# Kernel optimization log

Measured on AMD Instinct MI355X. Metric: run time of the kernel, lower is better.

## Reference

```python
import jax, jax.numpy as jnp
import numpy as np

B, FH, N, TIN = 8, 8, 2048, 5      # batch(time for LSTM), f_length, nodes, in_length
H1, H2 = 32, 64                    # traj_linear_hidden, lstm_encoder_size
NEG = -9e15

def setup_inputs() -> dict:
    key = jax.random.key(0)
    ks = jax.random.split(key, 12)
    s = lambda k, shape, fan: jax.random.normal(k, shape, jnp.float32) * (1.0 / np.sqrt(fan))
    return {
        "hist": jax.random.normal(ks[0], (B, FH, N, TIN), jnp.float32),
        "adj": jax.random.randint(ks[1], (B, 2, N, N), 0, 2, jnp.int32),
        "W1": s(ks[2], (H1, TIN * FH), TIN * FH),
        "b1": jnp.zeros((H1,), jnp.float32),
        "W_ih": s(ks[3], (4 * H2, H1), H1),
        "W_hh": s(ks[4], (4 * H2, H2), H2),
        "b_ih": jnp.zeros((4 * H2,), jnp.float32),
        "b_hh": jnp.zeros((4 * H2,), jnp.float32),
        "Wg": s(ks[5], (H2, H2), H2),
        "a_src": s(ks[6], (H2,), H2),
        "a_dst": s(ks[7], (H2,), H2),
    }

def _lstm(x, W_ih, W_hh, b_ih, b_hh):
    # x: [T, Nb, H1] (torch nn.LSTM seq-first); gate order i,f,g,o
    Nb = x.shape[1]
    h0 = jnp.zeros((Nb, H2), x.dtype)
    c0 = jnp.zeros((Nb, H2), x.dtype)
    def step(carry, xt):
        h, c = carry
        g = xt @ W_ih.T + b_ih + h @ W_hh.T + b_hh        # [Nb, 4*H2]
        i, f, gg, o = jnp.split(g, 4, axis=-1)
        c = jax.nn.sigmoid(f) * c + jax.nn.sigmoid(i) * jnp.tanh(gg)
        h = jax.nn.sigmoid(o) * jnp.tanh(c)
        return (h, c), h
    _, hs = jax.lax.scan(step, (h0, c0), x)
    return hs                                              # [T, Nb, H2]

def reference(hist, adj, W1, b1, W_ih, W_hh, b_ih, b_hh, Wg, a_src, a_dst):
    # hist.permute(0,2,3,1).flatten(2,3) -> [B, N, TIN*FH]
    x = jnp.transpose(hist, (0, 2, 3, 1)).reshape(B, N, TIN * FH)
    h1 = jax.nn.elu(x @ W1.T + b1)                         # [B, N, H1]
    hs = _lstm(h1, W_ih, W_hh, b_ih, b_hh)                 # [B, N, H2]
    # GAT over adj[:, -1]
    A = adj[:, -1, :, :] > 0                               # [B, N, N]
    Wh = hs @ Wg                                           # [B, N, H2]
    e = jax.nn.leaky_relu(
        (Wh @ a_src)[:, :, None] + (Wh @ a_dst)[:, None, :], 0.2)
    e = jnp.where(A, e, NEG)
    alpha = jax.nn.softmax(e, axis=-1)                     # [B, N, N]
    out = jax.nn.elu(jnp.einsum("bij,bjd->bid", alpha, Wh))
    return out
```

## Files before the change

kernel.cpp:

```cpp
#include <hip/hip_runtime.h>
#include <hip/hip_bf16.h>
#include <math.h>

#define BB 8
#define FH 8
#define NN 2048
#define TIN 5
#define H1 32
#define H2 64

typedef const void* cvp;
typedef __attribute__((ext_vector_type(8))) short short8;
typedef __attribute__((ext_vector_type(4))) float floatx4;

__device__ __forceinline__ float ldx(cvp p, int i, int bf) {
  if (bf) return __bfloat162float(((const __hip_bfloat16*)p)[i]);
  return ((const float*)p)[i];
}

__device__ __forceinline__ float4 ld4(cvp p, int i, int bf) {
  if (bf) {
    const __hip_bfloat162* q = (const __hip_bfloat162*)p;
    float2 a = __bfloat1622float2(q[(i >> 1)]);
    float2 b = __bfloat1622float2(q[(i >> 1) + 1]);
    return make_float4(a.x, a.y, b.x, b.y);
  }
  return ((const float4*)p)[i >> 2];
}

__device__ __forceinline__ float sigf(float x) {
  return 1.f / (1.f + __expf(-x));
}

__global__ void k_detect(const unsigned int* __restrict__ w, int* __restrict__ flag) {
  __shared__ int cnt;
  if (threadIdx.x == 0) cnt = 0;
  __syncthreads();
  int local = 0;
  for (int i = threadIdx.x; i < 1024; i += 256) {
    unsigned e = (w[i] >> 7) & 0xFFu;
    local += (e >= 100u && e <= 150u) ? 1 : 0;
  }
  atomicAdd(&cnt, local);
  __syncthreads();
  if (threadIdx.x == 0) *flag = (cnt > 700) ? 1 : 0;
}

__global__ void k_h1(cvp hist, cvp W1, cvp b1, float* __restrict__ h1,
                     const int* __restrict__ flagp) {
  __shared__ float w[H1 * TIN * FH];
  __shared__ float bb[H1];
  int bf = *flagp;
  int tid = threadIdx.x;
  for (int i = tid; i < H1 * TIN * FH; i += 256) w[i] = ldx(W1, i, bf);
  if (tid < H1) bb[tid] = ldx(b1, tid, bf);
  __syncthreads();
  int t = blockIdx.x >> 8;
  int n = ((blockIdx.x & 255) << 3) + (tid >> 5);
  int k = tid & 31;
  float acc = bb[k];
#pragma unroll
  for (int ti = 0; ti < TIN; ++ti) {
#pragma unroll
    for (int f = 0; f < FH; ++f) {
      acc += ldx(hist, (((t * FH + f) * NN + n) * TIN) + ti, bf) *
             w[k * (TIN * FH) + ti * FH + f];
    }
  }
  h1[((t * NN + n) * H1) + k] = (acc > 0.f) ? acc : expm1f(acc);
}

__global__ __launch_bounds__(256, 2) void k_lstm(
    const float* __restrict__ h1, cvp W_ih, cvp W_hh, cvp b_ih, cvp b_hh,
    float* __restrict__ hs, const int* __restrict__ flagp) {
  __shared__ __align__(16) float xh[4][96];
  __shared__ float gbuf[4][256];
  int bf = *flagp;
  int tid = threadIdx.x;
  int w = tid >> 6, lane = tid & 63;
  int g = (w << 6) + lane;
  int n0 = blockIdx.x << 2;
  int node_w = n0 + w;

  float wreg[96];
#pragma unroll
  for (int kq = 0; kq < 8; ++kq) {
    float4 v = ld4(W_ih, g * 32 + (kq << 2), bf);
    wreg[(kq << 2) + 0] = v.x; wreg[(kq << 2) + 1] = v.y;
    wreg[(kq << 2) + 2] = v.z; wreg[(kq << 2) + 3] = v.w;
  }
#pragma unroll
  for (int kq = 0; kq < 16; ++kq) {
    float4 v = ld4(W_hh, g * 64 + (kq << 2), bf);
    wreg[32 + (kq << 2) + 0] = v.x; wreg[32 + (kq << 2) + 1] = v.y;
    wreg[32 + (kq << 2) + 2] = v.z; wreg[32 + (kq << 2) + 3] = v.w;
  }
  float bias = ldx(b_ih, g, bf) + ldx(b_hh, g, bf);

  xh[w][32 + lane] = 0.f;
  float c = 0.f;

  for (int t = 0; t < BB; ++t) {
    if (lane < 32) xh[w][lane] = h1[((t * NN + node_w) * H1) + lane];
    __syncthreads();
    float acc[4] = {bias, bias, bias, bias};
    const float4* xq0 = (const float4*)xh[0];
    const float4* xq1 = (const float4*)xh[1];
    const float4* xq2 = (const float4*)xh[2];
    const float4* xq3 = (const float4*)xh[3];
#pragma unroll
    for (int kq = 0; kq < 24; ++kq) {
      float w0 = wreg[(kq << 2) + 0], w1 = wreg[(kq << 2) + 1];
      float w2 = wreg[(kq << 2) + 2], w3 = wreg[(kq << 2) + 3];
      float4 v0 = xq0[kq], v1 = xq1[kq], v2 = xq2[kq], v3 = xq3[kq];
      acc[0] += w0 * v0.x + w1 * v0.y + w2 * v0.z + w3 * v0.w;
      acc[1] += w0 * v1.x + w1 * v1.y + w2 * v1.z + w3 * v1.w;
      acc[2] += w0 * v2.x + w1 * v2.y + w2 * v2.z + w3 * v2.w;
      acc[3] += w0 * v3.x + w1 * v3.y + w2 * v3.z + w3 * v3.w;
    }
#pragma unroll
    for (int nd = 0; nd < 4; ++nd) gbuf[nd][g] = acc[nd];
    __syncthreads();
    float gi = gbuf[w][lane];
    float gf = gbuf[w][64 + lane];
    float gg = gbuf[w][128 + lane];
    float go = gbuf[w][192 + lane];
    c = sigf(gf) * c + sigf(gi) * tanhf(gg);
    float h = sigf(go) * tanhf(c);
    xh[w][32 + lane] = h;
    hs[((t * NN + node_w) * H2) + lane] = h;
    __syncthreads();
  }
}

__global__ __launch_bounds__(256) void k_gatprep(
    const float* __restrict__ hs, cvp Wg, cvp a_src, cvp a_dst,
    __hip_bfloat16* __restrict__ WhFr, float* __restrict__ sv,
    float* __restrict__ dv, const int* __restrict__ flagp) {
  __shared__ float wg[H2 * H2];
  __shared__ float tile[32][H2 + 1];
  int bf = *flagp;
  int tid = threadIdx.x;
  for (int i = tid; i < H2 * H2; i += 256) wg[i] = ldx(Wg, i, bf);
  __syncthreads();
  int wave = tid >> 6, lane = tid & 63;
  int b = blockIdx.x >> 6;
  int jt = blockIdx.x & 63;
  int j0 = jt << 5;
  float as = ldx(a_src, lane, bf);
  float ad = ldx(a_dst, lane, bf);
#pragma unroll
  for (int rr = 0; rr < 8; ++rr) {
    int jl = (wave << 3) + rr;
    int row = b * NN + j0 + jl;
    float hreg = hs[row * H2 + lane];
    float acc = 0.f;
#pragma unroll
    for (int k = 0; k < H2; ++k)
      acc += __shfl(hreg, k, 64) * wg[(k << 6) + lane];
    tile[jl][lane] = acc;
    float s = acc * as, d = acc * ad;
#pragma unroll
    for (int off = 32; off > 0; off >>= 1) {
      s += __shfl_xor(s, off, 64);
      d += __shfl_xor(d, off, 64);
    }
    if (lane == 0) { sv[row] = s; dv[row] = d; }
  }
  __syncthreads();
  int nt = tid >> 6, l = tid & 63;
  int q = l >> 4, m = l & 15;
  float v[8];
#pragma unroll
  for (int jj = 0; jj < 8; ++jj)
    v[jj] = tile[(q << 3) + jj][(nt << 4) + m];
  short8 fr;
#pragma unroll
  for (int p = 0; p < 4; ++p)
    ((__hip_bfloat162*)&fr)[p] =
        __float22bfloat162_rn(make_float2(v[2 * p], v[2 * p + 1]));
  size_t off = ((size_t)(b * 64 + jt) * 4 + nt) * 64 + l;
  ((short8*)WhFr)[off] = fr;
}

struct Stage {
  int4 a0, a1;
  float4 d0, d1;
  short8 b0, b1, b2, b3;
};

__device__ __forceinline__ Stage ld_stage(const int* arow, const float* drow,
                                          const short8* wf, int ks, int k0, int lane) {
  Stage s;
  int kb = ks * 32 + k0;
  s.a0 = *(const int4*)(arow + kb);
  s.a1 = *(const int4*)(arow + kb + 4);
  s.d0 = *(const float4*)(drow + kb);
  s.d1 = *(const float4*)(drow + kb + 4);
  const short8* base = wf + (size_t)ks * 256 + lane;
  s.b0 = base[0];
  s.b1 = base[64];
  s.b2 = base[128];
  s.b3 = base[192];
  return s;
}

__global__ __launch_bounds__(256, 3) void k_gat(
    const int* __restrict__ adj, const __hip_bfloat16* __restrict__ WhFr,
    const float* __restrict__ sv, const float* __restrict__ dv,
    void* __restrict__ out, const int* __restrict__ flagp) {
  __shared__ floatx4 abuf[3][4][64];
  __shared__ float sbuf[3][64];
  int bf = *flagp;
  int tid = threadIdx.x;
  int w = tid >> 6, lane = tid & 63;
  int b = blockIdx.x >> 7;
  int i0 = (blockIdx.x & 127) << 4;
  int q = lane >> 4, m = lane & 15;
  int i = i0 + m;
  float sva = sv[b * NN + i];
  const int* arow = adj + ((size_t)(b * 2 + 1) * NN + i) * NN;
  const float* drow = dv + b * NN;
  const short8* wf = ((const short8*)WhFr) + (size_t)b * 64 * 256;
  floatx4 acc0 = {0.f, 0.f, 0.f, 0.f};
  floatx4 acc1 = acc0, acc2 = acc0, acc3 = acc0;
  float S = 0.f;
  int k0 = q << 3;
  int ksb = w << 4;

  Stage s0 = ld_stage(arow, drow, wf, ksb + 0, k0, lane);
  Stage s1 = ld_stage(arow, drow, wf, ksb + 1, k0, lane);
#pragma unroll 2
  for (int ks = 0; ks < 16; ++ks) {
    int ksn = ksb + ((ks + 2 < 16) ? ks + 2 : 15);
    Stage nx = ld_stage(arow, drow, wf, ksn, k0, lane);
    int av[8] = {s0.a0.x, s0.a0.y, s0.a0.z, s0.a0.w,
                 s0.a1.x, s0.a1.y, s0.a1.z, s0.a1.w};
    float dd[8] = {s0.d0.x, s0.d0.y, s0.d0.z, s0.d0.w,
                   s0.d1.x, s0.d1.y, s0.d1.z, s0.d1.w};
    float pv[8];
#pragma unroll
    for (int jj = 0; jj < 8; ++jj) {
      float t = sva + dd[jj];
      float e = __expf(fmaxf(t, 0.2f * t));
      float p = (av[jj] != 0) ? e : 0.f;
      pv[jj] = p;
      S += p;
    }
    short8 afr;
#pragma unroll
    for (int p2 = 0; p2 < 4; ++p2)
      ((__hip_bfloat162*)&afr)[p2] =
          __float22bfloat162_rn(make_float2(pv[2 * p2], pv[2 * p2 + 1]));
    acc0 = __builtin_amdgcn_mfma_f32_16x16x32_bf16(afr, s0.b0, acc0, 0, 0, 0);
    acc1 = __builtin_amdgcn_mfma_f32_16x16x32_bf16(afr, s0.b1, acc1, 0, 0, 0);
    acc2 = __builtin_amdgcn_mfma_f32_16x16x32_bf16(afr, s0.b2, acc2, 0, 0, 0);
    acc3 = __builtin_amdgcn_mfma_f32_16x16x32_bf16(afr, s0.b3, acc3, 0, 0, 0);
    s0 = s1;
    s1 = nx;
  }
  S += __shfl_xor(S, 16, 64);
  S += __shfl_xor(S, 32, 64);
  if (w > 0) {
    abuf[w - 1][0][lane] = acc0;
    abuf[w - 1][1][lane] = acc1;
    abuf[w - 1][2][lane] = acc2;
    abuf[w - 1][3][lane] = acc3;
    sbuf[w - 1][lane] = S;
  }
  __syncthreads();
  if (w != 0) return;
#pragma unroll
  for (int ww = 0; ww < 3; ++ww) {
    acc0 += abuf[ww][0][lane];
    acc1 += abuf[ww][1][lane];
    acc2 += abuf[ww][2][lane];
    acc3 += abuf[ww][3][lane];
    S += sbuf[ww][lane];
  }
  float inv = 1.f / S;
  float ivr[4];
#pragma unroll
  for (int r = 0; r < 4; ++r) ivr[r] = __shfl(inv, (q << 2) + r, 64);

  floatx4 accs[4] = {acc0, acc1, acc2, acc3};
  if (bf) {
    __hip_bfloat16* o = (__hip_bfloat16*)out;
#pragma unroll
    for (int nt = 0; nt < 4; ++nt) {
#pragma unroll
      for (int r = 0; r < 4; ++r) {
        float v = accs[nt][r] * ivr[r];
        v = (v > 0.f) ? v : expm1f(v);
        int row = i0 + (q << 2) + r;
        o[((size_t)b * NN + row) * H2 + (nt << 4) + m] = __float2bfloat16(v);
      }
    }
  } else {
    float* o = (float*)out;
#pragma unroll
    for (int nt = 0; nt < 4; ++nt) {
#pragma unroll
      for (int r = 0; r < 4; ++r) {
        float v = accs[nt][r] * ivr[r];
        v = (v > 0.f) ? v : expm1f(v);
        int row = i0 + (q << 2) + r;
        o[((size_t)b * NN + row) * H2 + (nt << 4) + m] = v;
      }
    }
  }
}

extern "C" void kernel_launch(void* const* d_in, const int* in_sizes, int n_in,
                              void* d_out, int out_size, void* d_ws, size_t ws_size,
                              hipStream_t stream) {
  (void)in_sizes; (void)n_in; (void)out_size; (void)ws_size;
  cvp hist  = d_in[0];
  const int* adj = (const int*)d_in[1];
  cvp W1    = d_in[2];
  cvp b1    = d_in[3];
  cvp W_ih  = d_in[4];
  cvp W_hh  = d_in[5];
  cvp b_ih  = d_in[6];
  cvp b_hh  = d_in[7];
  cvp Wg    = d_in[8];
  cvp a_src = d_in[9];
  cvp a_dst = d_in[10];

  float* ws  = (float*)d_ws;
  float* h1  = ws;
  float* hs  = h1 + BB * NN * H1;
  __hip_bfloat16* WhFr = (__hip_bfloat16*)(hs + BB * NN * H2);
  float* sv  = hs + BB * NN * H2 + 524288;
  float* dv  = sv + BB * NN;
  int* flag  = (int*)(dv + BB * NN);

  k_detect<<<1, 256, 0, stream>>>((const unsigned int*)W_ih, flag);
  k_h1<<<2048, 256, 0, stream>>>(hist, W1, b1, h1, flag);
  k_lstm<<<512, 256, 0, stream>>>(h1, W_ih, W_hh, b_ih, b_hh, hs, flag);
  k_gatprep<<<512, 256, 0, stream>>>(hs, Wg, a_src, a_dst, WhFr, sv, dv, flag);
  k_gat<<<1024, 256, 0, stream>>>(adj, WhFr, sv, dv, d_out, flag);
}
```

Baseline: 432.7 us.

## Fuse input projection into LSTM and bitmask adjacency with MFMA row-sum in GAT

Folds the first linear+ELU layer into the LSTM kernel, computing each timestep's 32-wide input from hist inside the block and dropping the h1 intermediate buffer and one launch. In the GAT kernel, each block first packs its 16 adjacency rows into shared-memory bitmasks via wave ballots and stages dv in shared memory. The main loop then reads mask bits and dv from LDS instead of streaming int4 adjacency per step. The softmax denominator moves to an extra MFMA against a ones vector, and occupancy is raised to 4 blocks. The costs are an extra barrier per LSTM step, a shallower prefetch pipeline in the GAT loop, and a row sum now taken over bf16-rounded probabilities.

After: 467.2 us. 8.0% more time.

```diff
diff --git a/kernel.cpp b/kernel.cpp
--- a/kernel.cpp
+++ b/kernel.cpp
@@ -46,35 +46,14 @@
   if (threadIdx.x == 0) *flag = (cnt > 700) ? 1 : 0;
 }
 
-__global__ void k_h1(cvp hist, cvp W1, cvp b1, float* __restrict__ h1,
-                     const int* __restrict__ flagp) {
-  __shared__ float w[H1 * TIN * FH];
-  __shared__ float bb[H1];
-  int bf = *flagp;
-  int tid = threadIdx.x;
-  for (int i = tid; i < H1 * TIN * FH; i += 256) w[i] = ldx(W1, i, bf);
-  if (tid < H1) bb[tid] = ldx(b1, tid, bf);
-  __syncthreads();
-  int t = blockIdx.x >> 8;
-  int n = ((blockIdx.x & 255) << 3) + (tid >> 5);
-  int k = tid & 31;
-  float acc = bb[k];
-#pragma unroll
-  for (int ti = 0; ti < TIN; ++ti) {
-#pragma unroll
-    for (int f = 0; f < FH; ++f) {
-      acc += ldx(hist, (((t * FH + f) * NN + n) * TIN) + ti, bf) *
-             w[k * (TIN * FH) + ti * FH + f];
-    }
-  }
-  h1[((t * NN + n) * H1) + k] = (acc > 0.f) ? acc : expm1f(acc);
-}
-
 __global__ __launch_bounds__(256, 2) void k_lstm(
-    const float* __restrict__ h1, cvp W_ih, cvp W_hh, cvp b_ih, cvp b_hh,
+    cvp hist, cvp W1, cvp b1, cvp W_ih, cvp W_hh, cvp b_ih, cvp b_hh,
     float* __restrict__ hs, const int* __restrict__ flagp) {
   __shared__ __align__(16) float xh[4][96];
   __shared__ float gbuf[4][256];
+  __shared__ float W1s[H1][41];
+  __shared__ float b1s[H1];
+  __shared__ float xstage[4][40];
   int bf = *flagp;
   int tid = threadIdx.x;
   int w = tid >> 6, lane = tid & 63;
@@ -82,6 +61,9 @@
   int n0 = blockIdx.x << 2;
   int node_w = n0 + w;
 
+  for (int i = tid; i < H1 * 40; i += 256) W1s[i / 40][i % 40] = ldx(W1, i, bf);
+  if (tid < H1) b1s[tid] = ldx(b1, tid, bf);
+
   float wreg[96];
 #pragma unroll
   for (int kq = 0; kq < 8; ++kq) {
@@ -101,7 +83,19 @@
   float c = 0.f;
 
   for (int t = 0; t < BB; ++t) {
-    if (lane < 32) xh[w][lane] = h1[((t * NN + node_w) * H1) + lane];
+    if (tid < 160) {
+      int nd = tid / 40, r = tid % 40;
+      int ti = r >> 3, f = r & 7;
+      xstage[nd][r] = ldx(hist, ((t * FH + f) * NN + n0 + nd) * TIN + ti, bf);
+    }
+    __syncthreads();
+    if (tid < 128) {
+      int nd = tid >> 5, k = tid & 31;
+      float acc = b1s[k];
+#pragma unroll
+      for (int j = 0; j < 40; ++j) acc += W1s[k][j] * xstage[nd][j];
+      xh[nd][k] = (acc > 0.f) ? acc : expm1f(acc);
+    }
     __syncthreads();
     float acc[4] = {bias, bias, bias, bias};
     const float4* xq0 = (const float4*)xh[0];
@@ -183,90 +177,87 @@
   ((short8*)WhFr)[off] = fr;
 }
 
-struct Stage {
-  int4 a0, a1;
-  float4 d0, d1;
-  short8 b0, b1, b2, b3;
-};
-
-__device__ __forceinline__ Stage ld_stage(const int* arow, const float* drow,
-                                          const short8* wf, int ks, int k0, int lane) {
-  Stage s;
-  int kb = ks * 32 + k0;
-  s.a0 = *(const int4*)(arow + kb);
-  s.a1 = *(const int4*)(arow + kb + 4);
-  s.d0 = *(const float4*)(drow + kb);
-  s.d1 = *(const float4*)(drow + kb + 4);
-  const short8* base = wf + (size_t)ks * 256 + lane;
-  s.b0 = base[0];
-  s.b1 = base[64];
-  s.b2 = base[128];
-  s.b3 = base[192];
-  return s;
-}
-
-__global__ __launch_bounds__(256, 3) void k_gat(
+__global__ __launch_bounds__(256, 4) void k_gat(
     const int* __restrict__ adj, const __hip_bfloat16* __restrict__ WhFr,
     const float* __restrict__ sv, const float* __restrict__ dv,
     void* __restrict__ out, const int* __restrict__ flagp) {
-  __shared__ floatx4 abuf[3][4][64];
-  __shared__ float sbuf[3][64];
+  __shared__ __align__(16) float dv_s[NN];
+  __shared__ unsigned int msk[16 * 65];
+  __shared__ floatx4 abuf[3][5][64];
   int bf = *flagp;
   int tid = threadIdx.x;
   int w = tid >> 6, lane = tid & 63;
   int b = blockIdx.x >> 7;
   int i0 = (blockIdx.x & 127) << 4;
   int q = lane >> 4, m = lane & 15;
-  int i = i0 + m;
-  float sva = sv[b * NN + i];
-  const int* arow = adj + ((size_t)(b * 2 + 1) * NN + i) * NN;
-  const float* drow = dv + b * NN;
-  const short8* wf = ((const short8*)WhFr) + (size_t)b * 64 * 256;
+
+  for (int j = tid; j < NN; j += 256) dv_s[j] = dv[b * NN + j];
+  const int* adjb = adj + ((size_t)(b * 2 + 1) * NN + i0) * NN;
+#pragma unroll
+  for (int rr = 0; rr < 4; ++rr) {
+    int row = (w << 2) + rr;
+    const int* ar = adjb + (size_t)row * NN;
+#pragma unroll 8
+    for (int it = 0; it < 32; ++it) {
+      int v = ar[(it << 6) + lane];
+      unsigned long long bal = __ballot(v != 0);
+      if (lane == 0) {
+        msk[row * 65 + (it << 1)] = (unsigned)bal;
+        msk[row * 65 + (it << 1) + 1] = (unsigned)(bal >> 32);
+      }
+    }
+  }
+  float sva = sv[b * NN + i0 + m];
+  __syncthreads();
+
+  short8 ones;
+#pragma unroll
+  for (int p = 0; p < 8; ++p) ones[p] = (short)0x3F80;
+
+  const short8* base = ((const short8*)WhFr) + (size_t)b * 16384 + lane;
+  int ksb = w << 4, kse = ksb + 16;
   floatx4 acc0 = {0.f, 0.f, 0.f, 0.f};
-  floatx4 acc1 = acc0, acc2 = acc0, acc3 = acc0;
-  float S = 0.f;
-  int k0 = q << 3;
-  int ksb = w << 4;
-
-  Stage s0 = ld_stage(arow, drow, wf, ksb + 0, k0, lane);
-  Stage s1 = ld_stage(arow, drow, wf, ksb + 1, k0, lane);
-#pragma unroll 2
-  for (int ks = 0; ks < 16; ++ks) {
-    int ksn = ksb + ((ks + 2 < 16) ? ks + 2 : 15);
-    Stage nx = ld_stage(arow, drow, wf, ksn, k0, lane);
-    int av[8] = {s0.a0.x, s0.a0.y, s0.a0.z, s0.a0.w,
-                 s0.a1.x, s0.a1.y, s0.a1.z, s0.a1.w};
-    float dd[8] = {s0.d0.x, s0.d0.y, s0.d0.z, s0.d0.w,
-                   s0.d1.x, s0.d1.y, s0.d1.z, s0.d1.w};
+  floatx4 acc1 = acc0, acc2 = acc0, acc3 = acc0, accS = acc0;
+
+  short8 cb0 = base[(size_t)ksb * 256];
+  short8 cb1 = base[(size_t)ksb * 256 + 64];
+  short8 cb2 = base[(size_t)ksb * 256 + 128];
+  short8 cb3 = base[(size_t)ksb * 256 + 192];
+  for (int ks = ksb; ks < kse; ++ks) {
+    short8 b0 = cb0, b1 = cb1, b2 = cb2, b3 = cb3;
+    int ksn = (ks + 1 < kse) ? ks + 1 : ks;
+    cb0 = base[(size_t)ksn * 256];
+    cb1 = base[(size_t)ksn * 256 + 64];
+    cb2 = base[(size_t)ksn * 256 + 128];
+    cb3 = base[(size_t)ksn * 256 + 192];
+    unsigned mword = msk[m * 65 + ks];
+    float4 d0 = *(const float4*)&dv_s[(ks << 5) + (q << 3)];
+    float4 d1 = *(const float4*)&dv_s[(ks << 5) + (q << 3) + 4];
+    float dd[8] = {d0.x, d0.y, d0.z, d0.w, d1.x, d1.y, d1.z, d1.w};
     float pv[8];
 #pragma unroll
     for (int jj = 0; jj < 8; ++jj) {
       float t = sva + dd[jj];
       float e = __expf(fmaxf(t, 0.2f * t));
-      float p = (av[jj] != 0) ? e : 0.f;
-      pv[jj] = p;
-      S += p;
+      pv[jj] = ((mword >> ((q << 3) + jj)) & 1u) ? e : 0.f;
     }
     short8 afr;
 #pragma unroll
     for (int p2 = 0; p2 < 4; ++p2)
       ((__hip_bfloat162*)&afr)[p2] =
           __float22bfloat162_rn(make_float2(pv[2 * p2], pv[2 * p2 + 1]));
-    acc0 = __builtin_amdgcn_mfma_f32_16x16x32_bf16(afr, s0.b0, acc0, 0, 0, 0);
-    acc1 = __builtin_amdgcn_mfma_f32_16x16x32_bf16(afr, s0.b1, acc1, 0, 0, 0);
-    acc2 = __builtin_amdgcn_mfma_f32_16x16x32_bf16(afr, s0.b2, acc2, 0, 0, 0);
-    acc3 = __builtin_amdgcn_mfma_f32_16x16x32_bf16(afr, s0.b3, acc3, 0, 0, 0);
-    s0 = s1;
-    s1 = nx;
-  }
-  S += __shfl_xor(S, 16, 64);
-  S += __shfl_xor(S, 32, 64);
+    acc0 = __builtin_amdgcn_mfma_f32_16x16x32_bf16(afr, b0, acc0, 0, 0, 0);
+    acc1 = __builtin_amdgcn_mfma_f32_16x16x32_bf16(afr, b1, acc1, 0, 0, 0);
+    acc2 = __builtin_amdgcn_mfma_f32_16x16x32_bf16(afr, b2, acc2, 0, 0, 0);
+    acc3 = __builtin_amdgcn_mfma_f32_16x16x32_bf16(afr, b3, acc3, 0, 0, 0);
+    accS = __builtin_amdgcn_mfma_f32_16x16x32_bf16(afr, ones, accS, 0, 0, 0);
+  }
   if (w > 0) {
     abuf[w - 1][0][lane] = acc0;
     abuf[w - 1][1][lane] = acc1;
     abuf[w - 1][2][lane] = acc2;
     abuf[w - 1][3][lane] = acc3;
-    sbuf[w - 1][lane] = S;
+    abuf[w - 1][4][lane] = accS;
   }
   __syncthreads();
   if (w != 0) return;
@@ -276,38 +267,34 @@
     acc1 += abuf[ww][1][lane];
     acc2 += abuf[ww][2][lane];
     acc3 += abuf[ww][3][lane];
-    S += sbuf[ww][lane];
-  }
-  float inv = 1.f / S;
-  float ivr[4];
-#pragma unroll
-  for (int r = 0; r < 4; ++r) ivr[r] = __shfl(inv, (q << 2) + r, 64);
-
+    accS += abuf[ww][4][lane];
+  }
   floatx4 accs[4] = {acc0, acc1, acc2, acc3};
+  float inv[4];
+#pragma unroll
+  for (int r = 0; r < 4; ++r) inv[r] = 1.f / accS[r];
   if (bf) {
     __hip_bfloat16* o = (__hip_bfloat16*)out;
 #pragma unroll
-    for (int nt = 0; nt < 4; ++nt) {
+    for (int nt = 0; nt < 4; ++nt)
 #pragma unroll
       for (int r = 0; r < 4; ++r) {
-        float v = accs[nt][r] * ivr[r];
+        float v = accs[nt][r] * inv[r];
         v = (v > 0.f) ? v : expm1f(v);
         int row = i0 + (q << 2) + r;
         o[((size_t)b * NN + row) * H2 + (nt << 4) + m] = __float2bfloat16(v);
       }
-    }
   } else {
     float* o = (float*)out;
 #pragma unroll
-    for (int nt = 0; nt < 4; ++nt) {
+    for (int nt = 0; nt < 4; ++nt)
 #pragma unroll
       for (int r = 0; r < 4; ++r) {
-        float v = accs[nt][r] * ivr[r];
+        float v = accs[nt][r] * inv[r];
         v = (v > 0.f) ? v : expm1f(v);
         int row = i0 + (q << 2) + r;
         o[((size_t)b * NN + row) * H2 + (nt << 4) + m] = v;
       }
-    }
   }
 }
 
@@ -328,16 +315,14 @@
   cvp a_dst = d_in[10];
 
   float* ws  = (float*)d_ws;
-  float* h1  = ws;
-  float* hs  = h1 + BB * NN * H1;
+  float* hs  = ws;
   __hip_bfloat16* WhFr = (__hip_bfloat16*)(hs + BB * NN * H2);
   float* sv  = hs + BB * NN * H2 + 524288;
   float* dv  = sv + BB * NN;
   int* flag  = (int*)(dv + BB * NN);
 
   k_detect<<<1, 256, 0, stream>>>((const unsigned int*)W_ih, flag);
-  k_h1<<<2048, 256, 0, stream>>>(hist, W1, b1, h1, flag);
-  k_lstm<<<512, 256, 0, stream>>>(h1, W_ih, W_hh, b_ih, b_hh, hs, flag);
+  k_lstm<<<512, 256, 0, stream>>>(hist, W1, b1, W_ih, W_hh, b_ih, b_hh, hs, flag);
   k_gatprep<<<512, 256, 0, stream>>>(hs, Wg, a_src, a_dst, WhFr, sv, dv, flag);
   k_gat<<<1024, 256, 0, stream>>>(adj, WhFr, sv, dv, d_out, flag);
 }
```
